# Kernel tuning notes

Measured on AMD Instinct MI355X. Metric: run time of the kernel, lower is better.

The kernel has to match this reference:

```python
import jax, jax.numpy as jnp
import numpy as np

RMS_EPS = 1e-5


def setup_inputs() -> dict:
    key = jax.random.key(0)
    ks = jax.random.split(key, 7)
    B, N, D, H = 8, 1024, 1024, 4
    Dv = D // H
    s = lambda k, shp, fan: jax.random.normal(k, shp, jnp.float32) * (1.0 / np.sqrt(fan))
    return {
        "x": jax.random.normal(ks[0], (B, N, D), jnp.float32),
        "Wq": s(ks[1], (D, D), D),
        "Wk": s(ks[2], (D, D), D),
        "Wv": s(ks[3], (D, D), D),
        "Wbeta": s(ks[4], (D, H), D),
        "Wo": s(ks[5], (D, D), D),
        "g_norm": jnp.ones((Dv,), jnp.float32),
    }


def _l2norm(t):
    return t / jnp.linalg.norm(t, axis=-1, keepdims=True)


def _delta_rule(q, k, v, beta):
    # q,k: [B,H,N,Dk]; v: [B,H,N,Dv]; beta: [B,H,N]
    B, H, N, Dk = q.shape
    Dv = v.shape[-1]
    # time-major for scan: [N,B,H,D]
    qT = jnp.moveaxis(q, 2, 0)
    kT = jnp.moveaxis(k, 2, 0)
    vT = jnp.moveaxis(v, 2, 0)
    bT = jnp.moveaxis(beta, 2, 0)  # [N,B,H]

    def step(S, inp):
        q_t, k_t, v_t, b_t = inp  # [B,H,Dk], [B,H,Dk], [B,H,Dv], [B,H]
        pred = jnp.einsum('bhk,bhkv->bhv', k_t, S)
        err = (v_t - pred) * b_t[..., None]          # delta-rule error, scaled by beta
        S = S + jnp.einsum('bhk,bhv->bhkv', k_t, err)  # rank-1 state update
        o_t = jnp.einsum('bhk,bhkv->bhv', q_t, S)
        return S, o_t

    S0 = jnp.zeros((B, H, Dk, Dv), q.dtype)
    _, oT = jax.lax.scan(step, S0, (qT, kT, vT, bT))
    return jnp.moveaxis(oT, 0, 2)  # [B,H,N,Dv]


def reference(x, Wq, Wk, Wv, Wbeta, Wo, g_norm):
    B, N, D = x.shape
    H = Wbeta.shape[1]
    Dk = Wq.shape[1] // H
    Dv = Wv.shape[1] // H
    split = lambda t, d: t.reshape(B, N, H, d).transpose(0, 2, 1, 3)  # b n (h d) -> b h n d
    q = _l2norm(split(x @ Wq, Dk))
    k = _l2norm(split(x @ Wk, Dk))
    v = split(x @ Wv, Dv)
    beta = jax.nn.sigmoid(x @ Wbeta).transpose(0, 2, 1)  # [B,H,N]
    o = _delta_rule(q, k, v, beta)  # [B,H,N,Dv]
    # per-head RMSNorm over Dv
    o = o * jax.lax.rsqrt(jnp.mean(o * o, axis=-1, keepdims=True) + RMS_EPS) * g_norm
    o = o.transpose(0, 2, 1, 3).reshape(B, N, H * Dv)  # b h n d -> b n (h d)
    return o @ Wo
```

## Files before the change

### kernel.cpp

```cpp
#include <hip/hip_runtime.h>
#include <hip/hip_bf16.h>
#include <math.h>

typedef unsigned short u16;
typedef __attribute__((ext_vector_type(8))) __bf16 bf16x8;
typedef __attribute__((ext_vector_type(4))) float f32x4;

#define MFMA16 __builtin_amdgcn_mfma_f32_16x16x32_bf16

__device__ __forceinline__ float bf2f(unsigned int u) {
    union { unsigned int i; float f; } x;
    x.i = (u & 0xffffu) << 16;
    return x.f;
}
__device__ __forceinline__ u16 f2bf(float f) {
    unsigned int i = __float_as_uint(f);
    unsigned int r = (i + 0x7fffu + ((i >> 16) & 1u)) >> 16;
    return (u16)r;
}

__device__ __forceinline__ void gload_lds16(const void* g, void* l) {
    __builtin_amdgcn_global_load_lds((const __attribute__((address_space(1))) void*)g,
                                     (__attribute__((address_space(3))) void*)l, 16, 0, 0);
}

#define BARS() do { asm volatile("s_waitcnt lgkmcnt(0)" ::: "memory"); \
                    __builtin_amdgcn_s_barrier(); } while (0)

__global__ void detect_dtype(const unsigned* __restrict__ wq, int* __restrict__ flag)
{
    int lane = threadIdx.x;
    unsigned lo = wq[lane] & 0xffffu;
    unsigned e = (lo >> 7) & 0xffu;
    int m = (e >= 0x6e && e <= 0x7e) ? 1 : 0;
#pragma unroll
    for (int s = 1; s < 64; s <<= 1) m += __shfl_xor(m, s);
    if (lane == 0) flag[0] = (m >= 32) ? 0 : 1;
}

__global__ __launch_bounds__(256) void convert_vec(
    const void* __restrict__ src, u16* __restrict__ dst, int n, const int* __restrict__ flag)
{
    int stride = gridDim.x * 256;
    int i0 = blockIdx.x * 256 + threadIdx.x;
    if (*flag) {
        const float* s = (const float*)src;
        for (int i = i0; i < n; i += stride) dst[i] = f2bf(s[i]);
    } else {
        const u16* s = (const u16*)src;
        for (int i = i0; i < n; i += stride) dst[i] = s[i];
    }
}

__global__ __launch_bounds__(256) void transpose_cvt(
    const void* __restrict__ w0, const void* __restrict__ w1,
    const void* __restrict__ w2, const void* __restrict__ w3,
    u16* __restrict__ o0, u16* __restrict__ o1,
    u16* __restrict__ o2, u16* __restrict__ o3, const int* __restrict__ flag)
{
    const void* in; u16* out;
    switch (blockIdx.z) {
        case 0: in = w0; out = o0; break;
        case 1: in = w1; out = o1; break;
        case 2: in = w2; out = o2; break;
        default: in = w3; out = o3; break;
    }
    int n  = blockIdx.x * 64 + (threadIdx.x & 63);
    int kb = blockIdx.y * 32 + (threadIdx.x >> 6) * 8;
    u16 v[8];
    if (*flag) {
        const float* f = (const float*)in;
#pragma unroll
        for (int j = 0; j < 8; ++j) v[j] = f2bf(f[(size_t)(kb + j) * 1024 + n]);
    } else {
        const u16* s = (const u16*)in;
#pragma unroll
        for (int j = 0; j < 8; ++j) v[j] = s[(size_t)(kb + j) * 1024 + n];
    }
    uint4 pk;
    pk.x = (unsigned)v[0] | ((unsigned)v[1] << 16);
    pk.y = (unsigned)v[2] | ((unsigned)v[3] << 16);
    pk.z = (unsigned)v[4] | ((unsigned)v[5] << 16);
    pk.w = (unsigned)v[6] | ((unsigned)v[7] << 16);
    *(uint4*)(out + (size_t)n * 1024 + kb) = pk;
}

__global__ __launch_bounds__(256) void gemm_bt(
    const u16* __restrict__ A, const u16* __restrict__ BT, void* __restrict__ C,
    int M, int Nn, int K, const int* __restrict__ flag, int fp32_out)
{
    __shared__ alignas(16) u16 As[128 * 32];
    __shared__ alignas(16) u16 Bs[128 * 32];
    const int tid  = threadIdx.x;
    const int lane = tid & 63;
    const int wv   = tid >> 6;
    const int wm   = wv >> 1, wn = wv & 1;
    const int bm   = blockIdx.x * 128, bn = blockIdx.y * 128;
    const int fr   = lane & 15, fk = lane >> 4;

    f32x4 acc[4][4];
#pragma unroll
    for (int i = 0; i < 4; ++i)
#pragma unroll
        for (int j = 0; j < 4; ++j) acc[i][j] = (f32x4){0.f, 0.f, 0.f, 0.f};

    for (int k0 = 0; k0 < K; k0 += 32) {
        __syncthreads();
#pragma unroll
        for (int p = 0; p < 2; ++p) {
            int i = tid + p * 256;
            int r = i >> 2, kc = (i & 3) << 3;
            gload_lds16(A  + (size_t)(bm + r) * K + k0 + kc,
                        (char*)As + (size_t)(wv * 64 + p * 256) * 16);
            gload_lds16(BT + (size_t)(bn + r) * K + k0 + kc,
                        (char*)Bs + (size_t)(wv * 64 + p * 256) * 16);
        }
        __syncthreads();
        bf16x8 af[4], bfr[4];
#pragma unroll
        for (int mi = 0; mi < 4; ++mi)
            af[mi] = *(const bf16x8*)(As + (wm * 64 + mi * 16 + fr) * 32 + fk * 8);
#pragma unroll
        for (int ni = 0; ni < 4; ++ni)
            bfr[ni] = *(const bf16x8*)(Bs + (wn * 64 + ni * 16 + fr) * 32 + fk * 8);
#pragma unroll
        for (int mi = 0; mi < 4; ++mi)
#pragma unroll
            for (int ni = 0; ni < 4; ++ni)
                acc[mi][ni] = MFMA16(af[mi], bfr[ni], acc[mi][ni], 0, 0, 0);
    }
    bool f32st = fp32_out && (*flag);
    if (f32st) {
        float* Cf = (float*)C;
#pragma unroll
        for (int mi = 0; mi < 4; ++mi)
#pragma unroll
            for (int ni = 0; ni < 4; ++ni)
#pragma unroll
                for (int j = 0; j < 4; ++j) {
                    int row = bm + wm * 64 + mi * 16 + fk * 4 + j;
                    int col = bn + wn * 64 + ni * 16 + fr;
                    Cf[(size_t)row * Nn + col] = acc[mi][ni][j];
                }
    } else {
        u16* Cb = (u16*)C;
#pragma unroll
        for (int mi = 0; mi < 4; ++mi)
#pragma unroll
            for (int ni = 0; ni < 4; ++ni)
#pragma unroll
                for (int j = 0; j < 4; ++j) {
                    int row = bm + wm * 64 + mi * 16 + fk * 4 + j;
                    int col = bn + wn * 64 + ni * 16 + fr;
                    Cb[(size_t)row * Nn + col] = f2bf(acc[mi][ni][j]);
                }
    }
}

__global__ __launch_bounds__(256) void gemm_qkv(
    const u16* __restrict__ A, const u16* __restrict__ BT,
    u16* __restrict__ Qo, u16* __restrict__ Ko, u16* __restrict__ Vo)
{
    __shared__ alignas(16) u16 As[128 * 32];
    __shared__ alignas(16) u16 Bs[128 * 32];
    const int tid  = threadIdx.x;
    const int lane = tid & 63;
    const int wv   = tid >> 6;
    const int wm   = wv >> 1, wn = wv & 1;
    const int bm   = blockIdx.x * 128, bn = blockIdx.y * 128;
    const int fr   = lane & 15, fk = lane >> 4;

    f32x4 acc[4][4];
#pragma unroll
    for (int i = 0; i < 4; ++i)
#pragma unroll
        for (int j = 0; j < 4; ++j) acc[i][j] = (f32x4){0.f, 0.f, 0.f, 0.f};

    for (int k0 = 0; k0 < 1024; k0 += 32) {
        __syncthreads();
#pragma unroll
        for (int p = 0; p < 2; ++p) {
            int i = tid + p * 256;
            int r = i >> 2, kc = (i & 3) << 3;
            gload_lds16(A  + (size_t)(bm + r) * 1024 + k0 + kc,
                        (char*)As + (size_t)(wv * 64 + p * 256) * 16);
            gload_lds16(BT + (size_t)(bn + r) * 1024 + k0 + kc,
                        (char*)Bs + (size_t)(wv * 64 + p * 256) * 16);
        }
        __syncthreads();
        bf16x8 af[4], bfr[4];
#pragma unroll
        for (int mi = 0; mi < 4; ++mi)
            af[mi] = *(const bf16x8*)(As + (wm * 64 + mi * 16 + fr) * 32 + fk * 8);
#pragma unroll
        for (int ni = 0; ni < 4; ++ni)
            bfr[ni] = *(const bf16x8*)(Bs + (wn * 64 + ni * 16 + fr) * 32 + fk * 8);
#pragma unroll
        for (int mi = 0; mi < 4; ++mi)
#pragma unroll
            for (int ni = 0; ni < 4; ++ni)
                acc[mi][ni] = MFMA16(af[mi], bfr[ni], acc[mi][ni], 0, 0, 0);
    }
    const int seg = bn >> 10;
    u16* Cb = (seg == 0) ? Qo : (seg == 1) ? Ko : Vo;
    const int cb = bn & 1023;
#pragma unroll
    for (int mi = 0; mi < 4; ++mi)
#pragma unroll
        for (int ni = 0; ni < 4; ++ni)
#pragma unroll
            for (int j = 0; j < 4; ++j) {
                int row = bm + wm * 64 + mi * 16 + fk * 4 + j;
                int col = cb + wn * 64 + ni * 16 + fr;
                Cb[(size_t)row * 1024 + col] = f2bf(acc[mi][ni][j]);
            }
}

__global__ __launch_bounds__(256) void beta_kernel(
    const u16* __restrict__ x, const u16* __restrict__ Wb, float* __restrict__ beta)
{
    int row  = blockIdx.x * 4 + (threadIdx.x >> 6);
    int lane = threadIdx.x & 63;
    const u16* xr = x + (size_t)row * 1024;
    float a0 = 0.f, a1 = 0.f, a2 = 0.f, a3 = 0.f;
    for (int c = 0; c < 16; ++c) {
        int k = c * 64 + lane;
        float xv = bf2f(xr[k]);
        uint2 w = *(const uint2*)(Wb + (size_t)k * 4);
        a0 += xv * bf2f(w.x);
        a1 += xv * bf2f(w.x >> 16);
        a2 += xv * bf2f(w.y);
        a3 += xv * bf2f(w.y >> 16);
    }
#pragma unroll
    for (int m = 1; m < 64; m <<= 1) {
        a0 += __shfl_xor(a0, m); a1 += __shfl_xor(a1, m);
        a2 += __shfl_xor(a2, m); a3 += __shfl_xor(a3, m);
    }
    if (lane == 0) {
        int b = row >> 10, nn = row & 1023;
        beta[(size_t)(b * 4 + 0) * 1024 + nn] = 1.f / (1.f + expf(-a0));
        beta[(size_t)(b * 4 + 1) * 1024 + nn] = 1.f / (1.f + expf(-a1));
        beta[(size_t)(b * 4 + 2) * 1024 + nn] = 1.f / (1.f + expf(-a2));
        beta[(size_t)(b * 4 + 3) * 1024 + nn] = 1.f / (1.f + expf(-a3));
    }
}

__global__ __launch_bounds__(256) void l2norm_qk(u16* __restrict__ Q, u16* __restrict__ K)
{
    u16* base = blockIdx.y ? K : Q;
    int w    = blockIdx.x * 4 + (threadIdx.x >> 6);
    int lane = threadIdx.x & 63;
    u16* p = base + (size_t)(w >> 2) * 1024 + (w & 3) * 256 + lane * 4;
    uint2 u = *(const uint2*)p;
    float f0 = bf2f(u.x), f1 = bf2f(u.x >> 16), f2 = bf2f(u.y), f3 = bf2f(u.y >> 16);
    float ss = f0 * f0 + f1 * f1 + f2 * f2 + f3 * f3;
#pragma unroll
    for (int m = 1; m < 64; m <<= 1) ss += __shfl_xor(ss, m);
    float inv = rsqrtf(ss + 1e-20f);
    uint2 o;
    o.x = (unsigned)f2bf(f0 * inv) | ((unsigned)f2bf(f1 * inv) << 16);
    o.y = (unsigned)f2bf(f2 * inv) | ((unsigned)f2bf(f3 * inv) << 16);
    *(uint2*)p = o;
}

#define AP 65
__global__ __launch_bounds__(256, 2) void phaseA(
    const u16* __restrict__ Kb, const u16* __restrict__ Qb,
    const float* __restrict__ Bp,
    u16* __restrict__ M1hi, u16* __restrict__ M1lo,
    u16* KTg)
{
    const int bh = blockIdx.x >> 4, ch = blockIdx.x & 15;
    const int bq = bh >> 2, h = bh & 3;
    const int tid = threadIdx.x;
    const int w = tid >> 6, L = tid & 63, fr = L & 15, fk = L >> 4;

    __shared__ alignas(16) u16 Ks[64 * 264];
    __shared__ alignas(16) u16 Qs[64 * 264];
    __shared__ float bc[64];

    float* Af = (float*)Ks;
    float* Tf = (float*)(Ks + 8320);
    u16* TtH = Qs;
    u16* TtL = Qs + 64 * 72;
    u16* QKs = Qs + 2 * 64 * 72;

    const size_t crow = ((size_t)bq * 1024 + ch * 64) * 1024 + (size_t)h * 256;
#pragma unroll
    for (int i = 0; i < 8; ++i) {
        int row = i * 8 + (tid >> 5), c8 = (tid & 31) * 8;
        uint4 kv = *(const uint4*)(Kb + crow + (size_t)row * 1024 + c8);
        uint4 qv = *(const uint4*)(Qb + crow + (size_t)row * 1024 + c8);
        *(uint4*)(Ks + row * 264 + c8) = kv;
        *(uint4*)(Qs + row * 264 + c8) = qv;
    }
    if (tid < 64) bc[tid] = Bp[(size_t)bh * 1024 + ch * 64 + tid];
    __syncthreads();

    const size_t kbase = (size_t)(bh * 16 + ch) * 16384;
#pragma unroll
    for (int i = 0; i < 8; ++i) {
        int item = tid + i * 256;
        int t = item & 63, g = item >> 6;
        union { uint4 q; u16 u[8]; } U;
        U.q = *(const uint4*)(Ks + t * 264 + g * 8);
#pragma unroll
        for (int e = 0; e < 8; ++e)
            KTg[kbase + (size_t)(g * 8 + e) * 64 + t] = U.u[e];
    }

    f32x4 kk[4], qk[4];
#pragma unroll
    for (int n = 0; n < 4; ++n) { kk[n] = (f32x4){0,0,0,0}; qk[n] = (f32x4){0,0,0,0}; }
#pragma unroll
    for (int k0 = 0; k0 < 8; ++k0) {
        bf16x8 ak = *(const bf16x8*)(Ks + (w * 16 + fr) * 264 + k0 * 32 + fk * 8);
        bf16x8 aq = *(const bf16x8*)(Qs + (w * 16 + fr) * 264 + k0 * 32 + fk * 8);
#pragma unroll
        for (int n = 0; n < 4; ++n) {
            bf16x8 bk = *(const bf16x8*)(Ks + (n * 16 + fr) * 264 + k0 * 32 + fk * 8);
            kk[n] = MFMA16(ak, bk, kk[n], 0, 0, 0);
            qk[n] = MFMA16(aq, bk, qk[n], 0, 0, 0);
        }
    }
    __syncthreads();

#pragma unroll
    for (int n = 0; n < 4; ++n)
#pragma unroll
        for (int j = 0; j < 4; ++j) {
            int t = w * 16 + fk * 4 + j, s = n * 16 + fr;
            Af[t * AP + s] = (s < t) ? bc[t] * kk[n][j] : 0.f;
            QKs[t * 72 + s] = f2bf((s <= t) ? qk[n][j] : 0.f);
        }
    for (int i = tid; i < 64 * AP; i += 256) Tf[i] = 0.f;
    __syncthreads();

    {
        int j = w * 16 + fr;
        int p = fk;
        for (int t = 0; t < 64; ++t) {
            float acc = 0.f;
#pragma unroll
            for (int i = 0; i < 16; ++i) {
                int s = p + 4 * i;
                acc += Af[t * AP + s] * Tf[s * AP + j];
            }
            acc += __shfl_xor(acc, 16);
            acc += __shfl_xor(acc, 32);
            float val = ((t == j) ? 1.f : 0.f) - acc;
            if (p == 0) Tf[t * AP + j] = val;
        }
    }
    __syncthreads();

#pragma unroll
    for (int e = 0; e < 16; ++e) {
        int idx = tid + e * 256;
        int t = idx >> 6, s = idx & 63;
        float f = Tf[t * AP + s];
        u16 hh = f2bf(f);
        TtH[s * 72 + t] = hh;
        TtL[s * 72 + t] = f2bf(f - bf2f(hh));
    }
    __syncthreads();

    const size_t tb2 = (size_t)(bh * 16 + ch) * 4096;
    f32x4 accM[4];
#pragma unroll
    for (int ns = 0; ns < 4; ++ns) accM[ns] = (f32x4){0,0,0,0};
#pragma unroll
    for (int k0 = 0; k0 < 2; ++k0) {
        bf16x8 aq = *(const bf16x8*)(QKs + (w * 16 + fr) * 72 + k0 * 32 + fk * 8);
#pragma unroll
        for (int ns = 0; ns < 4; ++ns) {
            bf16x8 bh_ = *(const bf16x8*)(TtH + (ns * 16 + fr) * 72 + k0 * 32 + fk * 8);
            bf16x8 bl_ = *(const bf16x8*)(TtL + (ns * 16 + fr) * 72 + k0 * 32 + fk * 8);
            accM[ns] = MFMA16(aq, bh_, accM[ns], 0, 0, 0);
            accM[ns] = MFMA16(aq, bl_, accM[ns], 0, 0, 0);
        }
    }
#pragma unroll
    for (int ns = 0; ns < 4; ++ns)
#pragma unroll
        for (int j = 0; j < 4; ++j) {
            int t = w * 16 + fk * 4 + j, a = ns * 16 + fr;
            float v = accM[ns][j];
            u16 hh = f2bf(v);
            M1hi[tb2 + t * 64 + a] = hh;
            M1lo[tb2 + t * 64 + a] = f2bf(v - bf2f(hh));
        }

    asm volatile("s_waitcnt vmcnt(0)" ::: "memory");
#pragma unroll
    for (int nn = 0; nn < 4; ++nn) {
        bf16x8 af2[2];
#pragma unroll
        for (int k0 = 0; k0 < 2; ++k0)
            af2[k0] = *(const bf16x8*)(KTg + kbase
                        + (size_t)(w * 64 + nn * 16 + fr) * 64 + k0 * 32 + fk * 8);
        f32x4 acc2[4];
#pragma unroll
        for (int ns = 0; ns < 4; ++ns) acc2[ns] = (f32x4){0,0,0,0};
#pragma unroll
        for (int k0 = 0; k0 < 2; ++k0)
#pragma unroll
            for (int ns = 0; ns < 4; ++ns) {
                bf16x8 bh_ = *(const bf16x8*)(TtH + (ns * 16 + fr) * 72 + k0 * 32 + fk * 8);
                bf16x8 bl_ = *(const bf16x8*)(TtL + (ns * 16 + fr) * 72 + k0 * 32 + fk * 8);
                acc2[ns] = MFMA16(af2[k0], bh_, acc2[ns], 0, 0, 0);
                acc2[ns] = MFMA16(af2[k0], bl_, acc2[ns], 0, 0, 0);
            }
        asm volatile("s_waitcnt vmcnt(0)" ::: "memory");
#pragma unroll
        for (int ns = 0; ns < 4; ++ns)
#pragma unroll
            for (int j = 0; j < 4; ++j)
                KTg[kbase + (size_t)(w * 64 + nn * 16 + fk * 4 + j) * 64 + ns * 16 + fr]
                    = f2bf(acc2[ns][j]);
    }
}

#define WTP 72
#define SHP 264
__global__ __launch_bounds__(256, 1) void phaseB(
    const u16* __restrict__ Kb, const u16* __restrict__ Qb, u16* Vb,
    const float* __restrict__ Bp,
    const u16* __restrict__ M1hi, const u16* __restrict__ M1lo,
    const u16* __restrict__ Ktil)
{
    const int bh  = blockIdx.x & 31;
    const int dvb = blockIdx.x >> 5;
    const int bq = bh >> 2, h = bh & 3;
    const int tid = threadIdx.x;
    const int w = tid >> 6, L = tid & 63, fr = L & 15, fk = L >> 4;
    const int rl = L >> 5, cp = L & 31;

    __shared__ alignas(16) u16 Kl[64 * 256];
    __shared__ alignas(16) u16 Ql[64 * 256];
    __shared__ alignas(16) u16 S_hi[32 * SHP];
    __shared__ alignas(16) u16 S_lo[32 * SHP];
    __shared__ alignas(16) u16 W_T[32 * WTP];
    __shared__ float bc[1024];

    for (int i = tid; i < 32 * SHP; i += 256) { S_hi[i] = 0; S_lo[i] = 0; }
    for (int i = tid; i < 1024; i += 256) bc[i] = Bp[(size_t)bh * 1024 + i];

    const size_t rb = ((size_t)bq * 1024) * 1024 + (size_t)h * 256;

    f32x4 sreg[2][4];
#pragma unroll
    for (int n = 0; n < 2; ++n)
#pragma unroll
        for (int nn = 0; nn < 4; ++nn) sreg[n][nn] = (f32x4){0,0,0,0};

    bf16x8 m1h[2], m1l[2], ktf[2][4];
    u16 vr[2][4];

    auto stage_kq = [&](int c) {
        const size_t crow = rb + (size_t)(c * 64) * 1024;
#pragma unroll
        for (int i = 0; i < 8; ++i) {
            int rg = w * 16 + 2 * i + rl;
            int cu = cp ^ (rg & 7);
            gload_lds16(Kb + crow + (size_t)rg * 1024 + cu * 8,
                        (char*)Kl + (size_t)(w * 16 + 2 * i) * 512);
            gload_lds16(Qb + crow + (size_t)rg * 1024 + cu * 8,
                        (char*)Ql + (size_t)(w * 16 + 2 * i) * 512);
        }
    };
    auto pf_m1 = [&](int c) {
        const size_t mb = (size_t)(bh * 16 + c) * 4096 + (size_t)(w * 16 + fr) * 64 + fk * 8;
#pragma unroll
        for (int k0 = 0; k0 < 2; ++k0) {
            m1h[k0] = *(const bf16x8*)(M1hi + mb + k0 * 32);
            m1l[k0] = *(const bf16x8*)(M1lo + mb + k0 * 32);
        }
    };
    auto pf_ktf = [&](int c) {
        const size_t kb2 = (size_t)(bh * 16 + c) * 16384;
#pragma unroll
        for (int k0 = 0; k0 < 2; ++k0)
#pragma unroll
            for (int nn = 0; nn < 4; ++nn)
                ktf[k0][nn] = *(const bf16x8*)(Ktil + kb2
                              + (size_t)(w * 64 + nn * 16 + fr) * 64 + k0 * 32 + fk * 8);
    };
    auto pf_vr = [&](int c) {
        const size_t crow = rb + (size_t)(c * 64) * 1024;
#pragma unroll
        for (int n = 0; n < 2; ++n)
#pragma unroll
            for (int j = 0; j < 4; ++j)
                vr[n][j] = Vb[crow + (size_t)(w * 16 + fk * 4 + j) * 1024
                              + dvb * 32 + n * 16 + fr];
    };

    stage_kq(0); pf_m1(0); pf_ktf(0); pf_vr(0);
    __syncthreads();

    for (int c = 0; c < 16; ++c) {
        asm volatile("s_waitcnt vmcnt(0)" ::: "memory");
        f32x4 aPh[2], aPl[2], aOh[2], aOl[2];
#pragma unroll
        for (int n = 0; n < 2; ++n) {
            aPh[n] = (f32x4){0,0,0,0}; aPl[n] = (f32x4){0,0,0,0};
            aOh[n] = (f32x4){0,0,0,0}; aOl[n] = (f32x4){0,0,0,0};
        }
#pragma unroll
        for (int k0 = 0; k0 < 8; ++k0) {
            int ru = ((k0 * 4 + fk) ^ (fr & 7)) * 8;
            bf16x8 kqf = *(const bf16x8*)(Kl + (w * 16 + fr) * 256 + ru);
            bf16x8 qqf = *(const bf16x8*)(Ql + (w * 16 + fr) * 256 + ru);
#pragma unroll
            for (int n = 0; n < 2; ++n) {
                bf16x8 shi = *(const bf16x8*)(S_hi + (n * 16 + fr) * SHP + k0 * 32 + fk * 8);
                bf16x8 slo = *(const bf16x8*)(S_lo + (n * 16 + fr) * SHP + k0 * 32 + fk * 8);
                aPh[n] = MFMA16(kqf, shi, aPh[n], 0, 0, 0);
                aPl[n] = MFMA16(kqf, slo, aPl[n], 0, 0, 0);
                aOh[n] = MFMA16(qqf, shi, aOh[n], 0, 0, 0);
                aOl[n] = MFMA16(qqf, slo, aOl[n], 0, 0, 0);
            }
        }
        const size_t crow = rb + (size_t)(c * 64) * 1024;
#pragma unroll
        for (int n = 0; n < 2; ++n) {
            f32x4 accP = aPh[n] + aPl[n];
#pragma unroll
            for (int j = 0; j < 4; ++j) {
                int t = w * 16 + fk * 4 + j;
                W_T[(n * 16 + fr) * WTP + t] = f2bf(bc[c * 64 + t] * (bf2f(vr[n][j]) - accP[j]));
            }
        }
        if (c + 1 < 16) stage_kq(c + 1);
        BARS();
        bf16x8 wf[2][2];
#pragma unroll
        for (int n = 0; n < 2; ++n)
#pragma unroll
            for (int k0 = 0; k0 < 2; ++k0)
                wf[n][k0] = *(const bf16x8*)(W_T + (n * 16 + fr) * WTP + k0 * 32 + fk * 8);
        f32x4 accO[2];
#pragma unroll
        for (int n = 0; n < 2; ++n) {
            accO[n] = aOh[n] + aOl[n];
#pragma unroll
            for (int k0 = 0; k0 < 2; ++k0) {
                accO[n] = MFMA16(m1h[k0], wf[n][k0], accO[n], 0, 0, 0);
                accO[n] = MFMA16(m1l[k0], wf[n][k0], accO[n], 0, 0, 0);
            }
#pragma unroll
            for (int j = 0; j < 4; ++j)
                Vb[crow + (size_t)(w * 16 + fk * 4 + j) * 1024 + dvb * 32 + n * 16 + fr]
                    = f2bf(accO[n][j]);
        }
        if (c + 1 < 16) pf_m1(c + 1);
        f32x4 dS[2][4];
#pragma unroll
        for (int n = 0; n < 2; ++n)
#pragma unroll
            for (int nn = 0; nn < 4; ++nn) dS[n][nn] = (f32x4){0,0,0,0};
#pragma unroll
        for (int k0 = 0; k0 < 2; ++k0)
#pragma unroll
            for (int n = 0; n < 2; ++n)
#pragma unroll
                for (int nn = 0; nn < 4; ++nn)
                    dS[n][nn] = MFMA16(wf[n][k0], ktf[k0][nn], dS[n][nn], 0, 0, 0);
        if (c + 1 < 16) { pf_ktf(c + 1); pf_vr(c + 1); }
#pragma unroll
        for (int n = 0; n < 2; ++n)
#pragma unroll
            for (int nn = 0; nn < 4; ++nn) {
                sreg[n][nn] = sreg[n][nn] + dS[n][nn];
#pragma unroll
                for (int j = 0; j < 4; ++j) {
                    int idx = (n * 16 + fk * 4 + j) * SHP + (w * 64 + nn * 16 + fr);
                    float s = sreg[n][nn][j];
                    u16 hh = f2bf(s);
                    S_hi[idx] = hh;
                    S_lo[idx] = f2bf(s - bf2f(hh));
                }
            }
        BARS();
    }
}

__global__ __launch_bounds__(256) void rmsnorm_o(u16* V, const u16* __restrict__ gn)
{
    int w    = blockIdx.x * 4 + (threadIdx.x >> 6);
    int lane = threadIdx.x & 63;
    u16* p = V + (size_t)(w >> 2) * 1024 + (w & 3) * 256 + lane * 4;
    uint2 u = *(const uint2*)p;
    float f0 = bf2f(u.x), f1 = bf2f(u.x >> 16), f2 = bf2f(u.y), f3 = bf2f(u.y >> 16);
    float ss = f0 * f0 + f1 * f1 + f2 * f2 + f3 * f3;
#pragma unroll
    for (int m = 1; m < 64; m <<= 1) ss += __shfl_xor(ss, m);
    float sc = rsqrtf(ss * (1.0f / 256.0f) + 1e-5f);
    int d0 = lane * 4;
    uint2 gu = *(const uint2*)(gn + d0);
    float g0 = bf2f(gu.x), g1 = bf2f(gu.x >> 16), g2 = bf2f(gu.y), g3 = bf2f(gu.y >> 16);
    uint2 o;
    o.x = (unsigned)f2bf(f0 * sc * g0) | ((unsigned)f2bf(f1 * sc * g1) << 16);
    o.y = (unsigned)f2bf(f2 * sc * g2) | ((unsigned)f2bf(f3 * sc * g3) << 16);
    *(uint2*)p = o;
}

extern "C" void kernel_launch(void* const* d_in, const int* in_sizes, int n_in,
                              void* d_out, int out_size, void* d_ws, size_t ws_size,
                              hipStream_t stream)
{
    const void* x  = d_in[0];
    const void* Wq = d_in[1];
    const void* Wk = d_in[2];
    const void* Wv = d_in[3];
    const void* Wb = d_in[4];
    const void* Wo = d_in[5];
    const void* gn = d_in[6];

    char* ws = (char*)d_ws;
    const size_t OFF_FLAG = 0;
    const size_t OFF_WBC  = 4096;
    const size_t OFF_GNC  = OFF_WBC + 8192;
    const size_t OFF_XB   = OFF_GNC + 4096;
    const size_t OFF_WQT  = OFF_XB + 16777216;
    const size_t OFF_WKT  = OFF_WQT + 2097152;
    const size_t OFF_WVT  = OFF_WKT + 2097152;
    const size_t OFF_WOT  = OFF_WVT + 2097152;
    const size_t OFF_Q    = OFF_WOT + 2097152;
    const size_t OFF_K    = OFF_Q + 16777216;
    const size_t OFF_V    = OFF_K + 16777216;
    const size_t OFF_BP   = OFF_V + 16777216;

    const size_t OFF_M1H  = OFF_XB + 8388608;
    const size_t OFF_M1L  = OFF_XB + 12582912;

    int*   flag = (int*)(ws + OFF_FLAG);
    u16*   Wbc  = (u16*)(ws + OFF_WBC);
    u16*   gnc  = (u16*)(ws + OFF_GNC);
    u16*   Xb   = (u16*)(ws + OFF_XB);
    u16*   wqT  = (u16*)(ws + OFF_WQT);
    u16*   wkT  = (u16*)(ws + OFF_WKT);
    u16*   wvT  = (u16*)(ws + OFF_WVT);
    u16*   woT  = (u16*)(ws + OFF_WOT);
    u16*   Qb   = (u16*)(ws + OFF_Q);
    u16*   Kb   = (u16*)(ws + OFF_K);
    u16*   Vb   = (u16*)(ws + OFF_V);
    float* Bp   = (float*)(ws + OFF_BP);
    u16*   M1hi = (u16*)(ws + OFF_M1H);
    u16*   M1lo = (u16*)(ws + OFF_M1L);
    u16*   KTg  = (u16*)d_out;

    detect_dtype<<<1, 64, 0, stream>>>((const unsigned*)Wq, flag);
    convert_vec<<<2048, 256, 0, stream>>>(x, Xb, 8388608, flag);
    convert_vec<<<16, 256, 0, stream>>>(Wb, Wbc, 4096, flag);
    convert_vec<<<1, 256, 0, stream>>>(gn, gnc, 256, flag);
    transpose_cvt<<<dim3(16, 32, 4), 256, 0, stream>>>(Wq, Wk, Wv, Wo, wqT, wkT, wvT, woT, flag);

    gemm_qkv<<<dim3(64, 24), 256, 0, stream>>>(Xb, wqT, Qb, Kb, Vb);
    beta_kernel<<<2048, 256, 0, stream>>>(Xb, Wbc, Bp);
    l2norm_qk<<<dim3(8192, 2), 256, 0, stream>>>(Qb, Kb);

    phaseA<<<512, 256, 0, stream>>>(Kb, Qb, Bp, M1hi, M1lo, KTg);
    phaseB<<<256, 256, 0, stream>>>(Kb, Qb, Vb, Bp, M1hi, M1lo, KTg);

    rmsnorm_o<<<8192, 256, 0, stream>>>(Vb, gnc);
    gemm_bt<<<dim3(64, 8), 256, 0, stream>>>(Vb, woT, d_out, 8192, 1024, 1024, flag, 1);
}
```

Measured before the change: 256.5 us.

## Split phaseB state columns across 8 waves with 512-thread blocks

The recurrent phaseB kernel now launches 512 threads per block instead of 256. Each of the 8 waves owns a single 16-column half of the value slice rather than both halves. This halves the serial MFMA chain and register footprint per wave and doubles the waves available to hide latency in the sequential chunk loop. The per-iteration barriers are reorganised: a combined vmcnt/lgkmcnt barrier at loop top replaces the trailing barrier, and the next chunk's K/Q staging now starts after the W_T barrier. The cost is more LDS traffic for redundant K/Q fragment reads and a heavier synchronisation at the top of each iteration.

```diff
diff --git a/kernel.cpp b/kernel.cpp
--- a/kernel.cpp
+++ b/kernel.cpp
@@ -26,6 +26,8 @@
 
 #define BARS() do { asm volatile("s_waitcnt lgkmcnt(0)" ::: "memory"); \
                     __builtin_amdgcn_s_barrier(); } while (0)
+#define SYNCALL() do { asm volatile("s_waitcnt vmcnt(0) lgkmcnt(0)" ::: "memory"); \
+                       __builtin_amdgcn_s_barrier(); } while (0)
 
 __global__ void detect_dtype(const unsigned* __restrict__ wq, int* __restrict__ flag)
 {
@@ -424,7 +426,7 @@
 
 #define WTP 72
 #define SHP 264
-__global__ __launch_bounds__(256, 1) void phaseB(
+__global__ __launch_bounds__(512, 1) void phaseB(
     const u16* __restrict__ Kb, const u16* __restrict__ Qb, u16* Vb,
     const float* __restrict__ Bp,
     const u16* __restrict__ M1hi, const u16* __restrict__ M1lo,
@@ -434,7 +436,10 @@
     const int dvb = blockIdx.x >> 5;
     const int bq = bh >> 2, h = bh & 3;
     const int tid = threadIdx.x;
-    const int w = tid >> 6, L = tid & 63, fr = L & 15, fk = L >> 4;
+    const int wv8 = tid >> 6;
+    const int n   = wv8 >> 2;
+    const int wg  = wv8 & 3;
+    const int L = tid & 63, fr = L & 15, fk = L >> 4;
     const int rl = L >> 5, cp = L & 31;
 
     __shared__ alignas(16) u16 Kl[64 * 256];
@@ -444,34 +449,32 @@
     __shared__ alignas(16) u16 W_T[32 * WTP];
     __shared__ float bc[1024];
 
-    for (int i = tid; i < 32 * SHP; i += 256) { S_hi[i] = 0; S_lo[i] = 0; }
-    for (int i = tid; i < 1024; i += 256) bc[i] = Bp[(size_t)bh * 1024 + i];
+    for (int i = tid; i < 32 * SHP; i += 512) { S_hi[i] = 0; S_lo[i] = 0; }
+    for (int i = tid; i < 1024; i += 512) bc[i] = Bp[(size_t)bh * 1024 + i];
 
     const size_t rb = ((size_t)bq * 1024) * 1024 + (size_t)h * 256;
 
-    f32x4 sreg[2][4];
-#pragma unroll
-    for (int n = 0; n < 2; ++n)
-#pragma unroll
-        for (int nn = 0; nn < 4; ++nn) sreg[n][nn] = (f32x4){0,0,0,0};
+    f32x4 sreg[4];
+#pragma unroll
+    for (int nn = 0; nn < 4; ++nn) sreg[nn] = (f32x4){0,0,0,0};
 
     bf16x8 m1h[2], m1l[2], ktf[2][4];
-    u16 vr[2][4];
+    u16 vr[4];
 
     auto stage_kq = [&](int c) {
         const size_t crow = rb + (size_t)(c * 64) * 1024;
 #pragma unroll
-        for (int i = 0; i < 8; ++i) {
-            int rg = w * 16 + 2 * i + rl;
+        for (int i = 0; i < 4; ++i) {
+            int rg = wv8 * 8 + 2 * i + rl;
             int cu = cp ^ (rg & 7);
             gload_lds16(Kb + crow + (size_t)rg * 1024 + cu * 8,
-                        (char*)Kl + (size_t)(w * 16 + 2 * i) * 512);
+                        (char*)Kl + (size_t)(wv8 * 8 + 2 * i) * 512);
             gload_lds16(Qb + crow + (size_t)rg * 1024 + cu * 8,
-                        (char*)Ql + (size_t)(w * 16 + 2 * i) * 512);
+                        (char*)Ql + (size_t)(wv8 * 8 + 2 * i) * 512);
         }
     };
     auto pf_m1 = [&](int c) {
-        const size_t mb = (size_t)(bh * 16 + c) * 4096 + (size_t)(w * 16 + fr) * 64 + fk * 8;
+        const size_t mb = (size_t)(bh * 16 + c) * 4096 + (size_t)(wg * 16 + fr) * 64 + fk * 8;
 #pragma unroll
         for (int k0 = 0; k0 < 2; ++k0) {
             m1h[k0] = *(const bf16x8*)(M1hi + mb + k0 * 32);
@@ -485,105 +488,81 @@
 #pragma unroll
             for (int nn = 0; nn < 4; ++nn)
                 ktf[k0][nn] = *(const bf16x8*)(Ktil + kb2
-                              + (size_t)(w * 64 + nn * 16 + fr) * 64 + k0 * 32 + fk * 8);
+                              + (size_t)(wg * 64 + nn * 16 + fr) * 64 + k0 * 32 + fk * 8);
     };
     auto pf_vr = [&](int c) {
         const size_t crow = rb + (size_t)(c * 64) * 1024;
 #pragma unroll
-        for (int n = 0; n < 2; ++n)
-#pragma unroll
-            for (int j = 0; j < 4; ++j)
-                vr[n][j] = Vb[crow + (size_t)(w * 16 + fk * 4 + j) * 1024
-                              + dvb * 32 + n * 16 + fr];
+        for (int j = 0; j < 4; ++j)
+            vr[j] = Vb[crow + (size_t)(wg * 16 + fk * 4 + j) * 1024
+                          + dvb * 32 + n * 16 + fr];
     };
 
     stage_kq(0); pf_m1(0); pf_ktf(0); pf_vr(0);
-    __syncthreads();
 
     for (int c = 0; c < 16; ++c) {
-        asm volatile("s_waitcnt vmcnt(0)" ::: "memory");
-        f32x4 aPh[2], aPl[2], aOh[2], aOl[2];
-#pragma unroll
-        for (int n = 0; n < 2; ++n) {
-            aPh[n] = (f32x4){0,0,0,0}; aPl[n] = (f32x4){0,0,0,0};
-            aOh[n] = (f32x4){0,0,0,0}; aOl[n] = (f32x4){0,0,0,0};
-        }
+        SYNCALL();
+        f32x4 aPh = (f32x4){0,0,0,0}, aPl = (f32x4){0,0,0,0};
+        f32x4 aOh = (f32x4){0,0,0,0}, aOl = (f32x4){0,0,0,0};
 #pragma unroll
         for (int k0 = 0; k0 < 8; ++k0) {
             int ru = ((k0 * 4 + fk) ^ (fr & 7)) * 8;
-            bf16x8 kqf = *(const bf16x8*)(Kl + (w * 16 + fr) * 256 + ru);
-            bf16x8 qqf = *(const bf16x8*)(Ql + (w * 16 + fr) * 256 + ru);
-#pragma unroll
-            for (int n = 0; n < 2; ++n) {
-                bf16x8 shi = *(const bf16x8*)(S_hi + (n * 16 + fr) * SHP + k0 * 32 + fk * 8);
-                bf16x8 slo = *(const bf16x8*)(S_lo + (n * 16 + fr) * SHP + k0 * 32 + fk * 8);
-                aPh[n] = MFMA16(kqf, shi, aPh[n], 0, 0, 0);
-                aPl[n] = MFMA16(kqf, slo, aPl[n], 0, 0, 0);
-                aOh[n] = MFMA16(qqf, shi, aOh[n], 0, 0, 0);
-                aOl[n] = MFMA16(qqf, slo, aOl[n], 0, 0, 0);
+            bf16x8 kqf = *(const bf16x8*)(Kl + (wg * 16 + fr) * 256 + ru);
+            bf16x8 qqf = *(const bf16x8*)(Ql + (wg * 16 + fr) * 256 + ru);
+            bf16x8 shi = *(const bf16x8*)(S_hi + (n * 16 + fr) * SHP + k0 * 32 + fk * 8);
+            bf16x8 slo = *(const bf16x8*)(S_lo + (n * 16 + fr) * SHP + k0 * 32 + fk * 8);
+            aPh = MFMA16(kqf, shi, aPh, 0, 0, 0);
+            aPl = MFMA16(kqf, slo, aPl, 0, 0, 0);
+            aOh = MFMA16(qqf, shi, aOh, 0, 0, 0);
+            aOl = MFMA16(qqf, slo, aOl, 0, 0, 0);
+        }
+        const size_t crow = rb + (size_t)(c * 64) * 1024;
+        {
+            f32x4 accP = aPh + aPl;
+#pragma unroll
+            for (int j = 0; j < 4; ++j) {
+                int t = wg * 16 + fk * 4 + j;
+                W_T[(n * 16 + fr) * WTP + t] = f2bf(bc[c * 64 + t] * (bf2f(vr[j]) - accP[j]));
             }
         }
-        const size_t crow = rb + (size_t)(c * 64) * 1024;
-#pragma unroll
-        for (int n = 0; n < 2; ++n) {
-            f32x4 accP = aPh[n] + aPl[n];
+        BARS();
+        if (c + 1 < 16) stage_kq(c + 1);
+        bf16x8 wf[2];
+#pragma unroll
+        for (int k0 = 0; k0 < 2; ++k0)
+            wf[k0] = *(const bf16x8*)(W_T + (n * 16 + fr) * WTP + k0 * 32 + fk * 8);
+        f32x4 accO = aOh + aOl;
+#pragma unroll
+        for (int k0 = 0; k0 < 2; ++k0) {
+            accO = MFMA16(m1h[k0], wf[k0], accO, 0, 0, 0);
+            accO = MFMA16(m1l[k0], wf[k0], accO, 0, 0, 0);
+        }
+#pragma unroll
+        for (int j = 0; j < 4; ++j)
+            Vb[crow + (size_t)(wg * 16 + fk * 4 + j) * 1024 + dvb * 32 + n * 16 + fr]
+                = f2bf(accO[j]);
+        if (c + 1 < 16) pf_m1(c + 1);
+        f32x4 dS[4];
+#pragma unroll
+        for (int nn = 0; nn < 4; ++nn) dS[nn] = (f32x4){0,0,0,0};
+#pragma unroll
+        for (int k0 = 0; k0 < 2; ++k0)
+#pragma unroll
+            for (int nn = 0; nn < 4; ++nn)
+                dS[nn] = MFMA16(wf[k0], ktf[k0][nn], dS[nn], 0, 0, 0);
+        if (c + 1 < 16) { pf_ktf(c + 1); pf_vr(c + 1); }
+#pragma unroll
+        for (int nn = 0; nn < 4; ++nn) {
+            sreg[nn] = sreg[nn] + dS[nn];
 #pragma unroll
             for (int j = 0; j < 4; ++j) {
-                int t = w * 16 + fk * 4 + j;
-                W_T[(n * 16 + fr) * WTP + t] = f2bf(bc[c * 64 + t] * (bf2f(vr[n][j]) - accP[j]));
+                int idx = (n * 16 + fk * 4 + j) * SHP + (wg * 64 + nn * 16 + fr);
+                float s = sreg[nn][j];
+                u16 hh = f2bf(s);
+                S_hi[idx] = hh;
+                S_lo[idx] = f2bf(s - bf2f(hh));
             }
         }
-        if (c + 1 < 16) stage_kq(c + 1);
-        BARS();
-        bf16x8 wf[2][2];
-#pragma unroll
-        for (int n = 0; n < 2; ++n)
-#pragma unroll
-            for (int k0 = 0; k0 < 2; ++k0)
-                wf[n][k0] = *(const bf16x8*)(W_T + (n * 16 + fr) * WTP + k0 * 32 + fk * 8);
-        f32x4 accO[2];
-#pragma unroll
-        for (int n = 0; n < 2; ++n) {
-            accO[n] = aOh[n] + aOl[n];
-#pragma unroll
-            for (int k0 = 0; k0 < 2; ++k0) {
-                accO[n] = MFMA16(m1h[k0], wf[n][k0], accO[n], 0, 0, 0);
-                accO[n] = MFMA16(m1l[k0], wf[n][k0], accO[n], 0, 0, 0);
-            }
-#pragma unroll
-            for (int j = 0; j < 4; ++j)
-                Vb[crow + (size_t)(w * 16 + fk * 4 + j) * 1024 + dvb * 32 + n * 16 + fr]
-                    = f2bf(accO[n][j]);
-        }
-        if (c + 1 < 16) pf_m1(c + 1);
-        f32x4 dS[2][4];
-#pragma unroll
-        for (int n = 0; n < 2; ++n)
-#pragma unroll
-            for (int nn = 0; nn < 4; ++nn) dS[n][nn] = (f32x4){0,0,0,0};
-#pragma unroll
-        for (int k0 = 0; k0 < 2; ++k0)
-#pragma unroll
-            for (int n = 0; n < 2; ++n)
-#pragma unroll
-                for (int nn = 0; nn < 4; ++nn)
-                    dS[n][nn] = MFMA16(wf[n][k0], ktf[k0][nn], dS[n][nn], 0, 0, 0);
-        if (c + 1 < 16) { pf_ktf(c + 1); pf_vr(c + 1); }
-#pragma unroll
-        for (int n = 0; n < 2; ++n)
-#pragma unroll
-            for (int nn = 0; nn < 4; ++nn) {
-                sreg[n][nn] = sreg[n][nn] + dS[n][nn];
-#pragma unroll
-                for (int j = 0; j < 4; ++j) {
-                    int idx = (n * 16 + fk * 4 + j) * SHP + (w * 64 + nn * 16 + fr);
-                    float s = sreg[n][nn][j];
-                    u16 hh = f2bf(s);
-                    S_hi[idx] = hh;
-                    S_lo[idx] = f2bf(s - bf2f(hh));
-                }
-            }
-        BARS();
     }
 }
 
@@ -663,7 +642,7 @@
     l2norm_qk<<<dim3(8192, 2), 256, 0, stream>>>(Qb, Kb);
 
     phaseA<<<512, 256, 0, stream>>>(Kb, Qb, Bp, M1hi, M1lo, KTg);
-    phaseB<<<256, 256, 0, stream>>>(Kb, Qb, Vb, Bp, M1hi, M1lo, KTg);
+    phaseB<<<256, 512, 0, stream>>>(Kb, Qb, Vb, Bp, M1hi, M1lo, KTg);
 
     rmsnorm_o<<<8192, 256, 0, stream>>>(Vb, gnc);
     gemm_bt<<<dim3(64, 8), 256, 0, stream>>>(Vb, woT, d_out, 8192, 1024, 1024, flag, 1);
```

New measurement: 272.7 us. +6.3%, slower.
